# Performance work log

Measured on AMD Instinct MI355X. Metric: run time of the kernel, lower is better.

## Reference

```python
import jax, jax.numpy as jnp
import numpy as np

EMBED = 512  # scale uses embed_size**-0.5 per the original forward (NOT head_size)


def setup_inputs() -> dict:
    key = jax.random.key(0)
    k1, k2, k3, k4 = jax.random.split(key, 4)
    B, T, D, H = 8, 4096, EMBED, 64
    inputs = jax.random.normal(k1, (B, T, D), dtype=jnp.float32)
    Wq = jax.random.normal(k2, (D, H), dtype=jnp.float32) * (D ** -0.5)
    Wk = jax.random.normal(k3, (D, H), dtype=jnp.float32) * (D ** -0.5)
    Wv = jax.random.normal(k4, (D, H), dtype=jnp.float32) * (D ** -0.5)
    return {"inputs": inputs, "Wq": Wq, "Wk": Wk, "Wv": Wv}


def reference(inputs, Wq, Wk, Wv):
    # inputs: [B, T, D]; Wq/Wk/Wv: [D, H]
    B, T, D = inputs.shape
    q = inputs @ Wq  # [B, T, H]
    k = inputs @ Wk  # [B, T, H]
    v = inputs @ Wv  # [B, T, H]
    scale = jnp.asarray(D, inputs.dtype) ** -0.5  # original scales by embed_size**-0.5
    scores = jnp.einsum('bth,bsh->bts', q, k) * scale  # [B, T, T]
    causal = jnp.arange(T)[:, None] >= jnp.arange(T)[None, :]  # lower-triangular
    scores = jnp.where(causal, scores, jnp.asarray(-jnp.inf, scores.dtype))
    weights = jax.nn.softmax(scores, axis=-1)
    # dropout is identity in eval mode
    return weights @ v  # [B, T, H]
```

## Files before the change

### kernel.cpp

```cpp
#include <hip/hip_runtime.h>
#include <hip/hip_bf16.h>
#include <math.h>

#define TSEQ 4096
#define NB 8
#define DEM 512
#define HD 64
#define KP 66
#define VP 34
#define WIP 136
#define WIMG 26624
#define QSZ ((size_t)NB * TSEQ * HD)
#define SLOTS_PER_B 144

typedef __attribute__((ext_vector_type(8))) short short8;
typedef __attribute__((ext_vector_type(4))) short short4v;
typedef __attribute__((ext_vector_type(4))) float float4v;
typedef __attribute__((ext_vector_type(16))) float f32x16;

__device__ __forceinline__ short f2bf(float f) {
    union { float f; unsigned u; } v; v.f = f;
    unsigned r = v.u + 0x7fffu + ((v.u >> 16) & 1u);
    return (short)(r >> 16);
}

__device__ __forceinline__ short8 pack8(float4 a, float4 b) {
    union { short8 s; __hip_bfloat162 h[4]; } u;
    u.h[0] = __float22bfloat162_rn(make_float2(a.x, a.y));
    u.h[1] = __float22bfloat162_rn(make_float2(a.z, a.w));
    u.h[2] = __float22bfloat162_rn(make_float2(b.x, b.y));
    u.h[3] = __float22bfloat162_rn(make_float2(b.z, b.w));
    return u.s;
}

__device__ __forceinline__ int pkbf2(float x, float y) {
    union { __hip_bfloat162 h; int i; } u;
    u.h = __float22bfloat162_rn(make_float2(x, y));
    return u.i;
}

__device__ __forceinline__ short8 mk8(int a, int b, int c, int d) {
    union { short8 s; int i[4]; } u;
    u.i[0] = a; u.i[1] = b; u.i[2] = c; u.i[3] = d;
    return u.s;
}

__device__ __forceinline__ void gload_lds16(const void* g, void* l) {
    __builtin_amdgcn_global_load_lds(
        (const __attribute__((address_space(1))) unsigned int*)g,
        (__attribute__((address_space(3))) unsigned int*)l,
        16, 0, 0);
}

__device__ __host__ __forceinline__ int slot_base(int mq) {
    int a = mq >> 2, r = mq & 3;
    return (a + 1) * (2 * a + r);
}

__global__ __launch_bounds__(256) void wtr_kernel(
    const float* __restrict__ Wq, const float* __restrict__ Wk,
    const float* __restrict__ Wv, short* __restrict__ wimg)
{
    __shared__ float t[64][65];
    const int tid = threadIdx.x;
    const int kb = blockIdx.x;
    const int k0 = kb * 64;
    const int m = blockIdx.y;
    const int c = kb >> 1, half = kb & 1;
    const float* W = (m == 0) ? Wq : ((m == 1) ? Wk : Wv);
    const float sc = (m == 0) ? 0.044194173824159216f : 1.0f;

#pragma unroll
    for (int i = 0; i < 4; ++i) {
        int f = tid + 256 * i;
        int k = f >> 4, n4 = (f & 15) * 4;
        float4 wv = *(const float4*)&W[(k0 + k) * HD + n4];
        t[k][n4 + 0] = wv.x; t[k][n4 + 1] = wv.y;
        t[k][n4 + 2] = wv.z; t[k][n4 + 3] = wv.w;
    }
    __syncthreads();
#pragma unroll
    for (int i = 0; i < 4; ++i) {
        int f = tid + 256 * i;
        int n = f >> 4, k4 = (f & 15) * 4;
        short4v o;
        o[0] = f2bf(t[k4 + 0][n] * sc);
        o[1] = f2bf(t[k4 + 1][n] * sc);
        o[2] = f2bf(t[k4 + 2][n] * sc);
        o[3] = f2bf(t[k4 + 3][n] * sc);
        *(short4v*)&wimg[c * WIMG + (64 * m + n) * WIP + half * 64 + k4] = o;
    }
}

__global__ __launch_bounds__(256, 2) void qkv_mfma(
    const float* __restrict__ x, const short* __restrict__ wimg,
    short* __restrict__ q, short* __restrict__ k, short* __restrict__ vt)
{
    __shared__ alignas(16) short wlds[WIMG];

    const int tid = threadIdx.x;
    const int w = tid >> 6;
    const int l15 = tid & 15;
    const int quad = (tid >> 4) & 3;
    const int rbase = blockIdx.x * 64 + w * 16 + l15;

    const float* xr = x + (size_t)rbase * DEM;
    float4v acc[12] = {};

    for (int c = 0; c < 4; ++c) {
        __syncthreads();
        {
            const char* gsrc = (const char*)(wimg + c * WIMG) + tid * 16;
            char* ldst = (char*)wlds + tid * 16;
#pragma unroll
            for (int i = 0; i < 13; ++i)
                gload_lds16(gsrc + i * 4096, ldst + i * 4096);
        }
        __syncthreads();

#pragma unroll
        for (int ks = 0; ks < 4; ++ks) {
            const int k0 = c * 128 + ks * 32 + quad * 8;
            float4 xa = *(const float4*)&xr[k0];
            float4 xb = *(const float4*)&xr[k0 + 4];
            short8 xv = pack8(xa, xb);
            const int lk = ks * 32 + quad * 8;
#pragma unroll
            for (int mt = 0; mt < 12; ++mt) {
                short8 wf = *(const short8*)&wlds[(mt * 16 + l15) * WIP + lk];
                acc[mt] = __builtin_amdgcn_mfma_f32_16x16x32_bf16(wf, xv, acc[mt], 0, 0, 0);
            }
        }
    }

#pragma unroll
    for (int mt = 0; mt < 8; ++mt) {
        short* dst = (mt < 4) ? q : k;
        short4v o;
        o[0] = f2bf(acc[mt][0]); o[1] = f2bf(acc[mt][1]);
        o[2] = f2bf(acc[mt][2]); o[3] = f2bf(acc[mt][3]);
        *(short4v*)&dst[(size_t)rbase * HD + (mt & 3) * 16 + quad * 4] = o;
    }
    const int b = rbase >> 12, t = rbase & (TSEQ - 1);
#pragma unroll
    for (int mt = 8; mt < 12; ++mt) {
#pragma unroll
        for (int reg = 0; reg < 4; ++reg) {
            int d = (mt - 8) * 16 + quad * 4 + reg;
            vt[((size_t)(b * HD + d)) * TSEQ + t] = f2bf(acc[mt][reg]);
        }
    }
}

__global__ __launch_bounds__(64, 3) void flash_mfma(
    const short* __restrict__ qw, const short* __restrict__ kw,
    const short* __restrict__ vtw, float* __restrict__ out,
    float* __restrict__ pO, float* __restrict__ stS)
{
    __shared__ short kt[32 * KP];
    __shared__ short vl[64 * VP];

    const int lane = threadIdx.x;
    const int q5 = lane & 31;
    const int hi = lane >> 5;
    const int bx = blockIdx.x;
    const int b = bx & 7;
    const int r = bx >> 3;
    const int w = r & 3;
    const int idx = r >> 2;

    int mq, j;
    if (idx < 120) {
        int t = idx;
        mq = 31; j = 0;
#pragma unroll 1
        for (int mm = 31; mm >= 3; --mm) {
            int f = (mm + 1) >> 2;
            if (t < f) { mq = mm; j = t; break; }
            t -= f;
        }
    } else {
        int t = idx - 120;
        int kc = t >> 3, p = t & 7;
        mq = (30 - kc) - 4 * p;
        j = (mq + 1) >> 2;
    }
    const int r0 = mq * 128;
    const int ss0 = 16 * j;
    const int ssend = min(16 * (j + 1), 4 * mq + w + 1);
    const int slot = b * SLOTS_PER_B + slot_base(mq) + j;
    const int qrow = r0 + w * 32 + q5;

    short8 qf[4];
    {
        const short* qp = qw + ((size_t)(b * TSEQ + qrow)) * HD + hi * 8;
#pragma unroll
        for (int ks = 0; ks < 4; ++ks) qf[ks] = *(const short8*)(qp + ks * 16);
    }

    f32x16 O0 = {}, O1 = {};
    float l_lane = 0.f;

    const short* kbase = kw + (size_t)b * TSEQ * HD;
    const short* vbase = vtw + (size_t)b * HD * TSEQ;
    const int krow = lane >> 3, kc8 = (lane & 7) * 8;
    const int vrow = lane >> 2, vc8 = (lane & 3) * 8;

    short8 pk0, pk1, pk2, pk3, pv0, pv1, pv2, pv3;
    {
        const short* kg = kbase + (size_t)(ss0 * 32) * HD;
        const short* vg = vbase + ss0 * 32;
        pk0 = *(const short8*)(kg + (krow +  0) * HD + kc8);
        pk1 = *(const short8*)(kg + (krow +  8) * HD + kc8);
        pk2 = *(const short8*)(kg + (krow + 16) * HD + kc8);
        pk3 = *(const short8*)(kg + (krow + 24) * HD + kc8);
        pv0 = *(const short8*)(vg + (size_t)(vrow +  0) * TSEQ + vc8);
        pv1 = *(const short8*)(vg + (size_t)(vrow + 16) * TSEQ + vc8);
        pv2 = *(const short8*)(vg + (size_t)(vrow + 32) * TSEQ + vc8);
        pv3 = *(const short8*)(vg + (size_t)(vrow + 48) * TSEQ + vc8);
    }

    for (int ss = ss0; ss < ssend; ++ss) {
        __syncthreads();
        *(short8*)&kt[(krow +  0) * KP + kc8] = pk0;
        *(short8*)&kt[(krow +  8) * KP + kc8] = pk1;
        *(short8*)&kt[(krow + 16) * KP + kc8] = pk2;
        *(short8*)&kt[(krow + 24) * KP + kc8] = pk3;
        *(short8*)&vl[(vrow +  0) * VP + vc8] = pv0;
        *(short8*)&vl[(vrow + 16) * VP + vc8] = pv1;
        *(short8*)&vl[(vrow + 32) * VP + vc8] = pv2;
        *(short8*)&vl[(vrow + 48) * VP + vc8] = pv3;
        __syncthreads();

        if (ss + 1 < ssend) {
            const short* kg = kbase + (size_t)((ss + 1) * 32) * HD;
            const short* vg = vbase + (ss + 1) * 32;
            pk0 = *(const short8*)(kg + (krow +  0) * HD + kc8);
            pk1 = *(const short8*)(kg + (krow +  8) * HD + kc8);
            pk2 = *(const short8*)(kg + (krow + 16) * HD + kc8);
            pk3 = *(const short8*)(kg + (krow + 24) * HD + kc8);
            pv0 = *(const short8*)(vg + (size_t)(vrow +  0) * TSEQ + vc8);
            pv1 = *(const short8*)(vg + (size_t)(vrow + 16) * TSEQ + vc8);
            pv2 = *(const short8*)(vg + (size_t)(vrow + 32) * TSEQ + vc8);
            pv3 = *(const short8*)(vg + (size_t)(vrow + 48) * TSEQ + vc8);
        }

        f32x16 S = {};
#pragma unroll
        for (int ks = 0; ks < 4; ++ks) {
            short8 a = *(const short8*)&kt[q5 * KP + ks * 16 + hi * 8];
            S = __builtin_amdgcn_mfma_f32_32x32x16_bf16(a, qf[ks], S, 0, 0, 0);
        }

        if (ss * 32 + 31 > r0 + w * 32) {
#pragma unroll
            for (int reg = 0; reg < 16; ++reg) {
                int key = ss * 32 + (reg & 3) + 8 * (reg >> 2) + 4 * hi;
                if (key > qrow) S[reg] = -INFINITY;
            }
        }

        float p[16];
#pragma unroll
        for (int reg = 0; reg < 16; ++reg) {
            p[reg] = __expf(S[reg]);
            l_lane += p[reg];
        }
        int dd[4][2];
#pragma unroll
        for (int a = 0; a < 4; ++a) {
            dd[a][0] = pkbf2(p[4 * a + 0], p[4 * a + 1]);
            dd[a][1] = pkbf2(p[4 * a + 2], p[4 * a + 3]);
        }
        int ra0 = __shfl_xor(hi ? dd[0][0] : dd[1][0], 32, 64);
        int ra1 = __shfl_xor(hi ? dd[0][1] : dd[1][1], 32, 64);
        int rb0 = __shfl_xor(hi ? dd[2][0] : dd[3][0], 32, 64);
        int rb1 = __shfl_xor(hi ? dd[2][1] : dd[3][1], 32, 64);
        short8 PA0 = hi ? mk8(ra0, ra1, dd[1][0], dd[1][1])
                        : mk8(dd[0][0], dd[0][1], ra0, ra1);
        short8 PA1 = hi ? mk8(rb0, rb1, dd[3][0], dd[3][1])
                        : mk8(dd[2][0], dd[2][1], rb0, rb1);

#pragma unroll
        for (int kr = 0; kr < 2; ++kr) {
            short8 pa = kr ? PA1 : PA0;
            short8 v0 = *(const short8*)&vl[(q5)      * VP + kr * 16 + hi * 8];
            short8 v1 = *(const short8*)&vl[(32 + q5) * VP + kr * 16 + hi * 8];
            O0 = __builtin_amdgcn_mfma_f32_32x32x16_bf16(pa, v0, O0, 0, 0, 0);
            O1 = __builtin_amdgcn_mfma_f32_32x32x16_bf16(pa, v1, O1, 0, 0, 0);
        }
    }

    const float ltot = l_lane + __shfl_xor(l_lane, 32, 64);

    if (mq <= 3) {
        float inv = 1.0f / ltot;
#pragma unroll
        for (int reg = 0; reg < 16; ++reg) {
            int qloc = (reg & 3) + 8 * (reg >> 2) + 4 * hi;
            float ir = __shfl(inv, qloc, 64);
            size_t rowb = (size_t)(b * TSEQ + r0 + w * 32 + qloc) * HD + q5;
            out[rowb]      = O0[reg] * ir;
            out[rowb + 32] = O1[reg] * ir;
        }
    } else {
        float* dest = pO + ((size_t)slot * 128 + w * 32) * HD + q5;
#pragma unroll
        for (int reg = 0; reg < 16; ++reg) {
            int qloc = (reg & 3) + 8 * (reg >> 2) + 4 * hi;
            dest[(size_t)qloc * HD]      = O0[reg];
            dest[(size_t)qloc * HD + 32] = O1[reg];
        }
        if (hi == 0) stS[slot * 128 + w * 32 + q5] = ltot;
    }
}

__global__ __launch_bounds__(256) void merge_kernel(
    float* __restrict__ out, const float* __restrict__ pO,
    const float* __restrict__ stS)
{
    const int tid = threadIdx.x;
    const int bx = blockIdx.x;
    const int b = bx / 56, loc = bx - b * 56;
    const int t = 512 + loc * 64 + (tid >> 2);
    const int dq = (tid & 3) * 16;
    const int mq = t >> 7, rr = t & 127;
    const int nseg = (mq + 4) >> 2;
    const int sb = b * SLOTS_PER_B + slot_base(mq);

    float denom = 0.f;
    for (int s = 0; s < nseg; ++s) denom += stS[(sb + s) * 128 + rr];
    float inv = 1.0f / denom;

    float4 o[4] = {};
    for (int s = 0; s < nseg; ++s) {
        const float4* pp = (const float4*)
            &pO[((size_t)(sb + s) * 128 + rr) * HD + dq];
#pragma unroll
        for (int i = 0; i < 4; ++i) {
            float4 p = pp[i];
            o[i].x += p.x; o[i].y += p.y;
            o[i].z += p.z; o[i].w += p.w;
        }
    }
    float4* op = (float4*)&out[((size_t)b * TSEQ + t) * HD + dq];
#pragma unroll
    for (int i = 0; i < 4; ++i) {
        o[i].x *= inv; o[i].y *= inv; o[i].z *= inv; o[i].w *= inv;
        op[i] = o[i];
    }
}

extern "C" void kernel_launch(void* const* d_in, const int* in_sizes, int n_in,
                              void* d_out, int out_size, void* d_ws, size_t ws_size,
                              hipStream_t stream) {
    const float* x  = (const float*)d_in[0];
    const float* Wq = (const float*)d_in[1];
    const float* Wk = (const float*)d_in[2];
    const float* Wv = (const float*)d_in[3];
    float* out = (float*)d_out;

    short* q  = (short*)d_ws;
    short* k  = q + QSZ;
    short* vt = k + QSZ;
    short* wimg = vt + QSZ;
    float* pO = (float*)(wimg + 4 * WIMG);
    float* stS = pO + (size_t)NB * SLOTS_PER_B * 128 * HD;

    wtr_kernel<<<dim3(8, 3), 256, 0, stream>>>(Wq, Wk, Wv, wimg);
    qkv_mfma<<<dim3(NB * TSEQ / 64), 256, 0, stream>>>(x, wimg, q, k, vt);
    flash_mfma<<<dim3(NB * SLOTS_PER_B * 4), 64, 0, stream>>>(q, k, vt, out, pO, stS);
    merge_kernel<<<dim3(448), 256, 0, stream>>>(out, pO, stS);
}
```

Before: 157.7 us.

## Share K/V tiles across four waves per block and use exp2 softmax

```diff
diff --git a/kernel.cpp b/kernel.cpp
--- a/kernel.cpp
+++ b/kernel.cpp
@@ -68,7 +68,8 @@
     const int m = blockIdx.y;
     const int c = kb >> 1, half = kb & 1;
     const float* W = (m == 0) ? Wq : ((m == 1) ? Wk : Wv);
-    const float sc = (m == 0) ? 0.044194173824159216f : 1.0f;
+    const float sc = (m == 0) ? (0.044194173824159216f * 1.4426950408889634f)
+                              : 1.0f;
 
 #pragma unroll
     for (int i = 0; i < 4; ++i) {
@@ -152,22 +153,22 @@
     }
 }
 
-__global__ __launch_bounds__(64, 3) void flash_mfma(
+__global__ __launch_bounds__(256, 4) void flash_mfma(
     const short* __restrict__ qw, const short* __restrict__ kw,
     const short* __restrict__ vtw, float* __restrict__ out,
     float* __restrict__ pO, float* __restrict__ stS)
 {
-    __shared__ short kt[32 * KP];
-    __shared__ short vl[64 * VP];
-
-    const int lane = threadIdx.x;
+    __shared__ short kt[2][32 * KP];
+    __shared__ short vl[2][64 * VP];
+
+    const int tid = threadIdx.x;
+    const int w = tid >> 6;
+    const int lane = tid & 63;
     const int q5 = lane & 31;
     const int hi = lane >> 5;
     const int bx = blockIdx.x;
     const int b = bx & 7;
-    const int r = bx >> 3;
-    const int w = r & 3;
-    const int idx = r >> 2;
+    const int idx = bx >> 3;
 
     int mq, j;
     if (idx < 120) {
@@ -187,7 +188,8 @@
     }
     const int r0 = mq * 128;
     const int ss0 = 16 * j;
-    const int ssend = min(16 * (j + 1), 4 * mq + w + 1);
+    const int ssend = min(16 * (j + 1), 4 * mq + 4);
+    const int wlast = 4 * mq + w;
     const int slot = b * SLOTS_PER_B + slot_base(mq) + j;
     const int qrow = r0 + w * 32 + q5;
 
@@ -203,91 +205,74 @@
 
     const short* kbase = kw + (size_t)b * TSEQ * HD;
     const short* vbase = vtw + (size_t)b * HD * TSEQ;
-    const int krow = lane >> 3, kc8 = (lane & 7) * 8;
-    const int vrow = lane >> 2, vc8 = (lane & 3) * 8;
-
-    short8 pk0, pk1, pk2, pk3, pv0, pv1, pv2, pv3;
-    {
-        const short* kg = kbase + (size_t)(ss0 * 32) * HD;
-        const short* vg = vbase + ss0 * 32;
-        pk0 = *(const short8*)(kg + (krow +  0) * HD + kc8);
-        pk1 = *(const short8*)(kg + (krow +  8) * HD + kc8);
-        pk2 = *(const short8*)(kg + (krow + 16) * HD + kc8);
-        pk3 = *(const short8*)(kg + (krow + 24) * HD + kc8);
-        pv0 = *(const short8*)(vg + (size_t)(vrow +  0) * TSEQ + vc8);
-        pv1 = *(const short8*)(vg + (size_t)(vrow + 16) * TSEQ + vc8);
-        pv2 = *(const short8*)(vg + (size_t)(vrow + 32) * TSEQ + vc8);
-        pv3 = *(const short8*)(vg + (size_t)(vrow + 48) * TSEQ + vc8);
-    }
+    const int krow = tid >> 3, kc8 = (tid & 7) * 8;
+    const int vrow = tid >> 2, vc8 = (tid & 3) * 8;
+
+    short8 pk, pv;
+    pk = *(const short8*)(kbase + (size_t)(ss0 * 32 + krow) * HD + kc8);
+    pv = *(const short8*)(vbase + (size_t)vrow * TSEQ + ss0 * 32 + vc8);
 
     for (int ss = ss0; ss < ssend; ++ss) {
+        short* kb_ = kt[ss & 1];
+        short* vb_ = vl[ss & 1];
+        *(short8*)&kb_[krow * KP + kc8] = pk;
+        *(short8*)&vb_[vrow * VP + vc8] = pv;
         __syncthreads();
-        *(short8*)&kt[(krow +  0) * KP + kc8] = pk0;
-        *(short8*)&kt[(krow +  8) * KP + kc8] = pk1;
-        *(short8*)&kt[(krow + 16) * KP + kc8] = pk2;
-        *(short8*)&kt[(krow + 24) * KP + kc8] = pk3;
-        *(short8*)&vl[(vrow +  0) * VP + vc8] = pv0;
-        *(short8*)&vl[(vrow + 16) * VP + vc8] = pv1;
-        *(short8*)&vl[(vrow + 32) * VP + vc8] = pv2;
-        *(short8*)&vl[(vrow + 48) * VP + vc8] = pv3;
-        __syncthreads();
 
         if (ss + 1 < ssend) {
-            const short* kg = kbase + (size_t)((ss + 1) * 32) * HD;
-            const short* vg = vbase + (ss + 1) * 32;
-            pk0 = *(const short8*)(kg + (krow +  0) * HD + kc8);
-            pk1 = *(const short8*)(kg + (krow +  8) * HD + kc8);
-            pk2 = *(const short8*)(kg + (krow + 16) * HD + kc8);
-            pk3 = *(const short8*)(kg + (krow + 24) * HD + kc8);
-            pv0 = *(const short8*)(vg + (size_t)(vrow +  0) * TSEQ + vc8);
-            pv1 = *(const short8*)(vg + (size_t)(vrow + 16) * TSEQ + vc8);
-            pv2 = *(const short8*)(vg + (size_t)(vrow + 32) * TSEQ + vc8);
-            pv3 = *(const short8*)(vg + (size_t)(vrow + 48) * TSEQ + vc8);
-        }
-
-        f32x16 S = {};
-#pragma unroll
-        for (int ks = 0; ks < 4; ++ks) {
-            short8 a = *(const short8*)&kt[q5 * KP + ks * 16 + hi * 8];
-            S = __builtin_amdgcn_mfma_f32_32x32x16_bf16(a, qf[ks], S, 0, 0, 0);
-        }
-
-        if (ss * 32 + 31 > r0 + w * 32) {
+            pk = *(const short8*)(kbase + (size_t)((ss + 1) * 32 + krow) * HD + kc8);
+            pv = *(const short8*)(vbase + (size_t)vrow * TSEQ + (ss + 1) * 32 + vc8);
+        }
+
+        if (ss <= wlast) {
+            f32x16 S = {};
+            __builtin_amdgcn_s_setprio(1);
+#pragma unroll
+            for (int ks = 0; ks < 4; ++ks) {
+                short8 a = *(const short8*)&kb_[q5 * KP + ks * 16 + hi * 8];
+                S = __builtin_amdgcn_mfma_f32_32x32x16_bf16(a, qf[ks], S, 0, 0, 0);
+            }
+            __builtin_amdgcn_s_setprio(0);
+
+            if (ss * 32 + 31 > r0 + w * 32) {
+#pragma unroll
+                for (int reg = 0; reg < 16; ++reg) {
+                    int key = ss * 32 + (reg & 3) + 8 * (reg >> 2) + 4 * hi;
+                    if (key > qrow) S[reg] = -INFINITY;
+                }
+            }
+
+            float p[16];
 #pragma unroll
             for (int reg = 0; reg < 16; ++reg) {
-                int key = ss * 32 + (reg & 3) + 8 * (reg >> 2) + 4 * hi;
-                if (key > qrow) S[reg] = -INFINITY;
-            }
-        }
-
-        float p[16];
-#pragma unroll
-        for (int reg = 0; reg < 16; ++reg) {
-            p[reg] = __expf(S[reg]);
-            l_lane += p[reg];
-        }
-        int dd[4][2];
-#pragma unroll
-        for (int a = 0; a < 4; ++a) {
-            dd[a][0] = pkbf2(p[4 * a + 0], p[4 * a + 1]);
-            dd[a][1] = pkbf2(p[4 * a + 2], p[4 * a + 3]);
-        }
-        int ra0 = __shfl_xor(hi ? dd[0][0] : dd[1][0], 32, 64);
-        int ra1 = __shfl_xor(hi ? dd[0][1] : dd[1][1], 32, 64);
-        int rb0 = __shfl_xor(hi ? dd[2][0] : dd[3][0], 32, 64);
-        int rb1 = __shfl_xor(hi ? dd[2][1] : dd[3][1], 32, 64);
-        short8 PA0 = hi ? mk8(ra0, ra1, dd[1][0], dd[1][1])
-                        : mk8(dd[0][0], dd[0][1], ra0, ra1);
-        short8 PA1 = hi ? mk8(rb0, rb1, dd[3][0], dd[3][1])
-                        : mk8(dd[2][0], dd[2][1], rb0, rb1);
-
-#pragma unroll
-        for (int kr = 0; kr < 2; ++kr) {
-            short8 pa = kr ? PA1 : PA0;
-            short8 v0 = *(const short8*)&vl[(q5)      * VP + kr * 16 + hi * 8];
-            short8 v1 = *(const short8*)&vl[(32 + q5) * VP + kr * 16 + hi * 8];
-            O0 = __builtin_amdgcn_mfma_f32_32x32x16_bf16(pa, v0, O0, 0, 0, 0);
-            O1 = __builtin_amdgcn_mfma_f32_32x32x16_bf16(pa, v1, O1, 0, 0, 0);
+                p[reg] = __builtin_amdgcn_exp2f(S[reg]);
+                l_lane += p[reg];
+            }
+            int dd[4][2];
+#pragma unroll
+            for (int a = 0; a < 4; ++a) {
+                dd[a][0] = pkbf2(p[4 * a + 0], p[4 * a + 1]);
+                dd[a][1] = pkbf2(p[4 * a + 2], p[4 * a + 3]);
+            }
+            int ra0 = __shfl_xor(hi ? dd[0][0] : dd[1][0], 32, 64);
+            int ra1 = __shfl_xor(hi ? dd[0][1] : dd[1][1], 32, 64);
+            int rb0 = __shfl_xor(hi ? dd[2][0] : dd[3][0], 32, 64);
+            int rb1 = __shfl_xor(hi ? dd[2][1] : dd[3][1], 32, 64);
+            short8 PA0 = hi ? mk8(ra0, ra1, dd[1][0], dd[1][1])
+                            : mk8(dd[0][0], dd[0][1], ra0, ra1);
+            short8 PA1 = hi ? mk8(rb0, rb1, dd[3][0], dd[3][1])
+                            : mk8(dd[2][0], dd[2][1], rb0, rb1);
+
+            __builtin_amdgcn_s_setprio(1);
+#pragma unroll
+            for (int kr = 0; kr < 2; ++kr) {
+                short8 pa = kr ? PA1 : PA0;
+                short8 v0 = *(const short8*)&vb_[(q5)      * VP + kr * 16 + hi * 8];
+                short8 v1 = *(const short8*)&vb_[(32 + q5) * VP + kr * 16 + hi * 8];
+                O0 = __builtin_amdgcn_mfma_f32_32x32x16_bf16(pa, v0, O0, 0, 0, 0);
+                O1 = __builtin_amdgcn_mfma_f32_32x32x16_bf16(pa, v1, O1, 0, 0, 0);
+            }
+            __builtin_amdgcn_s_setprio(0);
         }
     }
 
@@ -369,6 +354,6 @@
 
     wtr_kernel<<<dim3(8, 3), 256, 0, stream>>>(Wq, Wk, Wv, wimg);
     qkv_mfma<<<dim3(NB * TSEQ / 64), 256, 0, stream>>>(x, wimg, q, k, vt);
-    flash_mfma<<<dim3(NB * SLOTS_PER_B * 4), 64, 0, stream>>>(q, k, vt, out, pO, stS);
+    flash_mfma<<<dim3(NB * SLOTS_PER_B), 256, 0, stream>>>(q, k, vt, out, pO, stS);
     merge_kernel<<<dim3(448), 256, 0, stream>>>(out, pO, stS);
 }
```

Measured after the change: 201.2 us. 1.28x slower.
